# Optimization experiments

Hardware: AMD Instinct MI355X
Metric: run time of the kernel (lower is better)

Reference implementation:

```python
import jax, jax.numpy as jnp
import numpy as np

T, B, D, H, L = 512, 64, 1024, 1024, 2
W_SCALE = 0.02  # keep tanh out of saturation


def setup_inputs() -> dict:
    key = jax.random.key(0)
    ks = jax.random.split(key, 7)
    return {
        "x": jax.random.normal(ks[0], (T, B, D), dtype=jnp.float32),
        "Wi": jax.random.normal(ks[1], (L, H, D), dtype=jnp.float32) * W_SCALE,
        "bi": jax.random.normal(ks[2], (L, H), dtype=jnp.float32) * W_SCALE,
        "Wh": jax.random.normal(ks[3], (L, H, H), dtype=jnp.float32) * W_SCALE,
        "bh": jax.random.normal(ks[4], (L, H), dtype=jnp.float32) * W_SCALE,
        "Wo": jax.random.normal(ks[5], (L, H, H), dtype=jnp.float32) * W_SCALE,
        "bo": jax.random.normal(ks[6], (L, H), dtype=jnp.float32) * W_SCALE,
    }


def reference(x, Wi, bi, Wh, bh, Wo, bo):
    # Faithful to the original: ONE hidden state shared across all layers,
    # overwritten by each RNNCell call within a timestep.
    num_layers = Wi.shape[0]
    batch = x.shape[1]
    hidden0 = jnp.zeros((batch, Wh.shape[-1]), dtype=x.dtype)

    def step(hidden, xt):
        out = xt
        for l in range(num_layers):
            # h = i2h(out) + h2h(hidden); o = h2o(h); new hidden = tanh(h)
            h = out @ Wi[l].T + bi[l] + hidden @ Wh[l].T + bh[l]  # [B,H]
            out = h @ Wo[l].T + bo[l]
            hidden = jnp.tanh(h)
        return hidden, out

    final_hidden, outs = jax.lax.scan(step, hidden0, x)  # outs: [T,B,H]
    return outs, final_hidden
```

## Files before the change

### kernel.cpp

```cpp
#include <hip/hip_runtime.h>
#include <cstdint>
#include <cstddef>

#define TT   512
#define NWG  256
#define SLOT 65536
#define SLOTB 262144
#define FINALOFF ((size_t)TT * (size_t)SLOT)

#define OFF_M     0
#define OFF_H0    2097152
#define OFF_TH0   (OFF_H0 + 131072)
#define OFF_TH1   (OFF_TH0 + 131072)
#define OFF_H1A   (OFF_TH1 + 131072)
#define OFF_H1B   (OFF_H1A + 131072)
#define OFF_B0    (OFF_H1B + 131072)
#define OFF_C1    (OFF_B0 + 4096)
#define OFF_FLAGS (OFF_C1 + 4096)

typedef _Float16 f16;
typedef unsigned long long ull;
typedef _Float16 v8h __attribute__((ext_vector_type(8)));
typedef float v4f __attribute__((ext_vector_type(4)));

union U2 { ull u[2]; v8h v; };
union P4 { f16 h[4]; ull u; };

__device__ __forceinline__ void st2(void* p, f16 v) {
  __hip_atomic_store((unsigned short*)p, __builtin_bit_cast(unsigned short, v),
                     __ATOMIC_RELAXED, __HIP_MEMORY_SCOPE_AGENT);
}
__device__ __forceinline__ ull ld8(const void* p) {
  return __hip_atomic_load((const ull*)p, __ATOMIC_RELAXED, __HIP_MEMORY_SCOPE_AGENT);
}
__device__ __forceinline__ void ld_frags(const f16* base, v8h out[8]) {
  ull u0[8], u1[8];
#pragma unroll
  for (int s = 0; s < 8; ++s) { const f16* p = base + s * 32; u0[s] = ld8(p); u1[s] = ld8(p + 4); }
#pragma unroll
  for (int s = 0; s < 8; ++s) { U2 c; c.u[0] = u0[s]; c.u[1] = u1[s]; out[s] = c.v; }
}

__device__ __forceinline__ float rcpf(float x) {
#if __has_builtin(__builtin_amdgcn_rcpf)
  return __builtin_amdgcn_rcpf(x);
#else
  return 1.0f / x;
#endif
}
__device__ __forceinline__ float tanhfast(float x) {
  x = fminf(fmaxf(x, -20.0f), 20.0f);
  const float u = __expf(-2.0f * x);
  return 1.0f - 2.0f * u * rcpf(1.0f + u);
}

__global__ void k_init(unsigned int* flags) {
  flags[threadIdx.x] = 0u;
}

__global__ void k_bias(const float* __restrict__ Wi, const float* __restrict__ bi,
                       const float* __restrict__ bh, const float* __restrict__ bo,
                       float* __restrict__ b0, float* __restrict__ c1) {
  const int i = blockIdx.x * 256 + threadIdx.x;
  const float* row = Wi + 1048576 + (size_t)i * 1024;
  float s = 0.f;
  for (int k = 0; k < 1024; k += 4) {
    const float4 w = *(const float4*)&row[k];
    const float4 v = *(const float4*)&bo[k];
    s += w.x * v.x + w.y * v.y + w.z * v.z + w.w * v.w;
  }
  c1[i] = s + bi[1024 + i] + bh[1024 + i];
  b0[i] = bi[i] + bh[i];
}

__global__ __launch_bounds__(256) void k_gemm_M(const float* __restrict__ Wi,
                                                const float* __restrict__ Wo,
                                                f16* __restrict__ Mh) {
  const float* A = Wi + 1048576;
  const float* B = Wo;
  __shared__ float As[16][68];
  __shared__ float Bs[16][68];
  const int bi = blockIdx.x >> 4, bj = blockIdx.x & 15;
  const int i0 = bi * 64, d0 = bj * 64;
  const int ti = threadIdx.x >> 4, tj = threadIdx.x & 15;
  float acc[4][4] = {};
  for (int kc = 0; kc < 1024; kc += 16) {
    const int r = threadIdx.x >> 2, cg = (threadIdx.x & 3) << 2;
    const float4 av = *(const float4*)&A[(size_t)(i0 + r) * 1024 + kc + cg];
    As[cg + 0][r] = av.x; As[cg + 1][r] = av.y; As[cg + 2][r] = av.z; As[cg + 3][r] = av.w;
    const int c2 = threadIdx.x >> 4, dg = (threadIdx.x & 15) << 2;
    const float4 bv = *(const float4*)&B[(size_t)(kc + c2) * 1024 + d0 + dg];
    *(float4*)&Bs[c2][dg] = bv;
    __syncthreads();
#pragma unroll
    for (int kk = 0; kk < 16; ++kk) {
      float a[4], b[4];
#pragma unroll
      for (int q = 0; q < 4; ++q) { a[q] = As[kk][ti * 4 + q]; b[q] = Bs[kk][tj * 4 + q]; }
#pragma unroll
      for (int p = 0; p < 4; ++p)
#pragma unroll
        for (int q = 0; q < 4; ++q) acc[p][q] += a[p] * b[q];
    }
    __syncthreads();
  }
#pragma unroll
  for (int p = 0; p < 4; ++p)
#pragma unroll
    for (int q = 0; q < 4; ++q)
      Mh[(size_t)(i0 + ti * 4 + p) * 1024 + (size_t)(d0 + tj * 4 + q)] = (f16)acc[p][q];
}

__global__ __launch_bounds__(256, 1) void k_z1(const float* __restrict__ x,
                                               const float* __restrict__ Wi,
                                               const float* __restrict__ b0p,
                                               float* __restrict__ dout) {
  const int t = blockIdx.x;
  const int tid = threadIdx.x, l = tid & 63, w = tid >> 6;
  const int lj = l & 15, lk = l >> 4;
  __shared__ __align__(16) f16 XL[64 * 1032];
  const float* xt = x + (size_t)t * SLOT;
  for (int u = tid; u < 16384; u += 256) {
    const int b = u >> 8, c4 = (u & 255) << 2;
    const float4 v = *(const float4*)&xt[(size_t)b * 1024 + c4];
    P4 p; p.h[0] = (f16)v.x; p.h[1] = (f16)v.y; p.h[2] = (f16)v.z; p.h[3] = (f16)v.w;
    *(ull*)&XL[b * 1032 + c4] = p.u;
  }
  __syncthreads();
  for (int jt = 0; jt < 16; ++jt) {
    const int jb = w * 256 + jt * 16;
    v4f acc[4] = {{0.f,0.f,0.f,0.f},{0.f,0.f,0.f,0.f},{0.f,0.f,0.f,0.f},{0.f,0.f,0.f,0.f}};
    for (int ks = 0; ks < 32; ++ks) {
      const int k0 = ks * 32 + lk * 8;
      const float* p = &Wi[(size_t)(jb + lj) * 1024 + k0];
      const float4 a = *(const float4*)p, b = *(const float4*)(p + 4);
      const v8h wf = {(f16)a.x,(f16)a.y,(f16)a.z,(f16)a.w,
                      (f16)b.x,(f16)b.y,(f16)b.z,(f16)b.w};
#pragma unroll
      for (int bt = 0; bt < 4; ++bt) {
        const v8h xf = *(const v8h*)&XL[(bt * 16 + lj) * 1032 + k0];
        acc[bt] = __builtin_amdgcn_mfma_f32_16x16x32_f16(xf, wf, acc[bt], 0, 0, 0);
      }
    }
    const float bias = b0p[jb + lj];
#pragma unroll
    for (int bt = 0; bt < 4; ++bt)
#pragma unroll
      for (int q = 0; q < 4; ++q) {
        const int b = bt * 16 + lk * 4 + q;
        f16* dst = (f16*)((char*)dout + (size_t)t * SLOTB + (size_t)(b >> 4) * 65536
                          + (size_t)(b & 15) * 2048) + (jb + lj);
        *dst = (f16)(acc[bt][q] + bias);
      }
  }
}

__global__ __launch_bounds__(256, 1) void k_rnn(
    const float* __restrict__ Wh, const float* __restrict__ Wo,
    const float* __restrict__ bo,
    char* __restrict__ ws, float* __restrict__ dout)
{
  const f16* Mh = (const f16*)(ws + OFF_M);
  f16* h0h  = (f16*)(ws + OFF_H0);
  f16* th0h = (f16*)(ws + OFF_TH0);
  f16* th1h = (f16*)(ws + OFF_TH1);
  f16* h1r[2] = { (f16*)(ws + OFF_H1A), (f16*)(ws + OFF_H1B) };
  const float* c1p = (const float*)(ws + OFF_C1);
  unsigned int* flags = (unsigned int*)(ws + OFF_FLAGS);

  const int wg = blockIdx.x;
  const int bq = wg & 3;
  const int jt = wg >> 2;
  const int j0 = jt * 16;
  const int tid = threadIdx.x;
  const int l = tid & 63, w = tid >> 6;
  const int lj = l & 15, lk = l >> 4;
  const int rb = tid >> 4, rj = tid & 15;
  unsigned int* gf = flags + bq * 64;

  __shared__ __align__(16) char WLb[4 * 32768];
  __shared__ float red[1024];

  {
    const float* srcs[3] = { Wh, Wh + 1048576, Wo + 1048576 };
    const int mi[3] = { 0, 2, 3 };
#pragma unroll
    for (int m = 0; m < 3; ++m) {
      const float* src = srcs[m];
      for (int u = tid; u < 4096; u += 256) {
        const int j = u >> 8, c4 = (u & 255) << 2;
        const float4 v = *(const float4*)&src[(size_t)(j0 + j) * 1024 + c4];
        P4 p; p.h[0] = (f16)v.x; p.h[1] = (f16)v.y; p.h[2] = (f16)v.z; p.h[3] = (f16)v.w;
        *(ull*)(WLb + mi[m] * 32768 + ((c4 >> 3) << 8) + (j << 4) + ((c4 & 4) << 1)) = p.u;
      }
    }
    for (int u = tid; u < 2048; u += 256) {
      const int j = u >> 7, c8 = (u & 127) << 3;
      const v8h mv = *(const v8h*)&Mh[(size_t)(j0 + j) * 1024 + c8];
      *(v8h*)(WLb + 32768 + ((c8 >> 3) << 8) + (j << 4)) = mv;
    }
  }
  const float c1v = c1p[j0 + rj];
  const float bo1v = bo[1024 + j0 + rj];
  __syncthreads();

  const size_t actbase = (size_t)(bq * 16 + lj) * 1024 + (size_t)(w * 256 + lk * 8);
  const int redw = w * 256 + lk * 64 + lj;
  const size_t rdst = (size_t)(bq * 16 + rb) * 1024 + (size_t)(j0 + rj);
  const int fbase = ((w * 32 + lk) << 8) + (lj << 4);

  auto wfrag = [&](int m, int s) -> v8h {
    return *(const v8h*)(WLb + m * 32768 + fbase + (s << 10));
  };
  auto zptr = [&](int t) -> const f16* {
    return (const f16*)((const char*)dout + (size_t)t * SLOTB + (size_t)bq * 65536
                        + (size_t)rb * 2048) + (j0 + rj);
  };
  auto reduce4 = [&](v4f a) -> float {
    __syncthreads();
#pragma unroll
    for (int q = 0; q < 4; ++q) red[redw + q * 16] = a[q];
    __syncthreads();
    return red[tid] + red[256 + tid] + red[512 + tid] + red[768 + tid];
  };
  auto pollge = [&](unsigned int ph) {
    if (tid < 64)
      while (__hip_atomic_load(&gf[tid], __ATOMIC_RELAXED, __HIP_MEMORY_SCOPE_AGENT) < ph)
        __builtin_amdgcn_s_sleep(1);
    __syncthreads();
    asm volatile("" ::: "memory");
  };
  auto setflag = [&](unsigned int ph) {
    if (tid == 0)
      __hip_atomic_store(&gf[jt], ph, __ATOMIC_RELAXED, __HIP_MEMORY_SCOPE_AGENT);
  };

  float zv = (float)(*zptr(0));
  v8h thf[8];

  for (int t = 0; t < TT; ++t) {
    const bool R = (t > 0);

    v4f accA = {0.f, 0.f, 0.f, 0.f};
    if (R) {
#pragma unroll
      for (int s = 0; s < 8; ++s)
        accA = __builtin_amdgcn_mfma_f32_16x16x32_f16(thf[s], wfrag(0, s), accA, 0, 0, 0);
    }
    const float h0 = reduce4(accA) + zv;
    st2(&h0h[rdst], (f16)h0);
    st2(&th0h[rdst], (f16)tanhfast(h0));

    v8h hrf[8];
    if (R) ld_frags(h1r[(t - 1) & 1] + actbase, hrf);
    float zn = 0.f;
    if (t + 1 < TT) zn = (float)(*zptr(t + 1));

    if (t == 0)            { asm volatile("s_waitcnt vmcnt(1)"  ::: "memory"); }
    else if (t == TT - 1)  { asm volatile("s_waitcnt vmcnt(16)" ::: "memory"); }
    else                   { asm volatile("s_waitcnt vmcnt(17)" ::: "memory"); }
    __syncthreads();
    setflag(2u * t + 1u);

    float oval = 0.f;
    if (R) {
      asm volatile("s_waitcnt vmcnt(0)" ::: "memory");
      v4f aa = {0.f, 0.f, 0.f, 0.f};
#pragma unroll
      for (int s = 0; s < 8; ++s)
        aa = __builtin_amdgcn_mfma_f32_16x16x32_f16(hrf[s], wfrag(3, s), aa, 0, 0, 0);
      oval = reduce4(aa) + bo1v;
    }
    pollge(2u * t + 1u);

    v8h g0f[8], t0f[8];
    ld_frags(h0h + actbase, g0f);
    ld_frags(th0h + actbase, t0f);
    v4f aM = {0.f, 0.f, 0.f, 0.f}, aW = {0.f, 0.f, 0.f, 0.f};
#pragma unroll
    for (int s = 0; s < 8; ++s) {
      aM = __builtin_amdgcn_mfma_f32_16x16x32_f16(g0f[s], wfrag(1, s), aM, 0, 0, 0);
      aW = __builtin_amdgcn_mfma_f32_16x16x32_f16(t0f[s], wfrag(2, s), aW, 0, 0, 0);
    }
    const float h1 = reduce4(aM + aW) + c1v;
    const float th1v = tanhfast(h1);
    st2(&h1r[t & 1][rdst], (f16)h1);
    st2(&th1h[rdst], (f16)th1v);
    if (R) dout[(size_t)(t - 1) * SLOT + rdst] = oval;
    if (t == TT - 1) dout[FINALOFF + rdst] = th1v;

    if (t == 0)            { asm volatile("s_waitcnt vmcnt(0)" ::: "memory"); }
    else if (t == TT - 1)  { asm volatile("s_waitcnt vmcnt(2)" ::: "memory"); }
    else                   { asm volatile("s_waitcnt vmcnt(1)" ::: "memory"); }
    __syncthreads();
    setflag(2u * t + 2u);
    pollge(2u * t + 2u);

    if (t + 1 < TT) ld_frags(th1h + actbase, thf);
    zv = zn;
  }

  {
    v8h hrf[8];
    ld_frags(h1r[(TT - 1) & 1] + actbase, hrf);
    v4f aa = {0.f, 0.f, 0.f, 0.f};
#pragma unroll
    for (int s = 0; s < 8; ++s)
      aa = __builtin_amdgcn_mfma_f32_16x16x32_f16(hrf[s], wfrag(3, s), aa, 0, 0, 0);
    dout[(size_t)(TT - 1) * SLOT + rdst] = reduce4(aa) + bo1v;
  }
}

extern "C" void kernel_launch(void* const* d_in, const int* in_sizes, int n_in,
                              void* d_out, int out_size, void* d_ws, size_t ws_size,
                              hipStream_t stream) {
  (void)in_sizes; (void)n_in; (void)out_size; (void)ws_size;
  const float* x  = (const float*)d_in[0];
  const float* Wi = (const float*)d_in[1];
  const float* bi = (const float*)d_in[2];
  const float* Wh = (const float*)d_in[3];
  const float* bh = (const float*)d_in[4];
  const float* Wo = (const float*)d_in[5];
  const float* bo = (const float*)d_in[6];
  char* ws = (char*)d_ws;
  float* out = (float*)d_out;

  k_init<<<1, 256, 0, stream>>>((unsigned int*)(ws + OFF_FLAGS));
  k_bias<<<4, 256, 0, stream>>>(Wi, bi, bh, bo, (float*)(ws + OFF_B0), (float*)(ws + OFF_C1));
  k_gemm_M<<<256, 256, 0, stream>>>(Wi, Wo, (f16*)(ws + OFF_M));
  k_z1<<<512, 256, 0, stream>>>(x, Wi, (const float*)(ws + OFF_B0), out);
  k_rnn<<<NWG, 256, 0, stream>>>(Wh, Wo, bo, ws, out);
}
```

Measured before the change: 6.856 ms.

## Replace flag barriers with tagged fp16 data polling and double-buffered activations

Drops the per-group flag arrays and the two flag-based barrier phases per timestep. Each fp16 activation now carries a 2-bit timestep tag in its low mantissa bits, and consumers spin on the data itself until every fragment holds the expected tag. Activation buffers are double-buffered and initialised to an invalid tag, and the output projection store moves earlier. This removes the global flag round trips and the __syncthreads/flag latency on the recurrent critical path, at the cost of two mantissa bits of precision and heavier polling traffic.

```diff
diff --git a/kernel.cpp b/kernel.cpp
--- a/kernel.cpp
+++ b/kernel.cpp
@@ -8,15 +8,11 @@
 #define SLOTB 262144
 #define FINALOFF ((size_t)TT * (size_t)SLOT)
 
-#define OFF_M     0
-#define OFF_H0    2097152
-#define OFF_TH0   (OFF_H0 + 131072)
-#define OFF_TH1   (OFF_TH0 + 131072)
-#define OFF_H1A   (OFF_TH1 + 131072)
-#define OFF_H1B   (OFF_H1A + 131072)
-#define OFF_B0    (OFF_H1B + 131072)
-#define OFF_C1    (OFF_B0 + 4096)
-#define OFF_FLAGS (OFF_C1 + 4096)
+#define OFF_M    0
+#define OFF_X    2097152
+#define XB(i)    (OFF_X + (i) * 131072)
+#define OFF_B0   (OFF_X + 1048576)
+#define OFF_C1   (OFF_B0 + 4096)
 
 typedef _Float16 f16;
 typedef unsigned long long ull;
@@ -33,12 +29,11 @@
 __device__ __forceinline__ ull ld8(const void* p) {
   return __hip_atomic_load((const ull*)p, __ATOMIC_RELAXED, __HIP_MEMORY_SCOPE_AGENT);
 }
-__device__ __forceinline__ void ld_frags(const f16* base, v8h out[8]) {
-  ull u0[8], u1[8];
-#pragma unroll
-  for (int s = 0; s < 8; ++s) { const f16* p = base + s * 32; u0[s] = ld8(p); u1[s] = ld8(p + 4); }
-#pragma unroll
-  for (int s = 0; s < 8; ++s) { U2 c; c.u[0] = u0[s]; c.u[1] = u1[s]; out[s] = c.v; }
+
+__device__ __forceinline__ f16 tagf(float v, unsigned tag) {
+  unsigned short b = __builtin_bit_cast(unsigned short, (f16)v);
+  b = (unsigned short)((b & 0xFFFCu) | (tag & 3u));
+  return __builtin_bit_cast(f16, b);
 }
 
 __device__ __forceinline__ float rcpf(float x) {
@@ -54,8 +49,9 @@
   return 1.0f - 2.0f * u * rcpf(1.0f + u);
 }
 
-__global__ void k_init(unsigned int* flags) {
-  flags[threadIdx.x] = 0u;
+__global__ void k_init(uint2* p) {
+  const uint2 v = { 0x00020002u, 0x00020002u };
+  p[(size_t)blockIdx.x * 256 + threadIdx.x] = v;
 }
 
 __global__ void k_bias(const float* __restrict__ Wi, const float* __restrict__ bi,
@@ -161,12 +157,11 @@
     char* __restrict__ ws, float* __restrict__ dout)
 {
   const f16* Mh = (const f16*)(ws + OFF_M);
-  f16* h0h  = (f16*)(ws + OFF_H0);
-  f16* th0h = (f16*)(ws + OFF_TH0);
-  f16* th1h = (f16*)(ws + OFF_TH1);
-  f16* h1r[2] = { (f16*)(ws + OFF_H1A), (f16*)(ws + OFF_H1B) };
+  f16* h0b[2]  = { (f16*)(ws + XB(0)), (f16*)(ws + XB(1)) };
+  f16* th0b[2] = { (f16*)(ws + XB(2)), (f16*)(ws + XB(3)) };
+  f16* h1b[2]  = { (f16*)(ws + XB(4)), (f16*)(ws + XB(5)) };
+  f16* th1b[2] = { (f16*)(ws + XB(6)), (f16*)(ws + XB(7)) };
   const float* c1p = (const float*)(ws + OFF_C1);
-  unsigned int* flags = (unsigned int*)(ws + OFF_FLAGS);
 
   const int wg = blockIdx.x;
   const int bq = wg & 3;
@@ -176,7 +171,6 @@
   const int l = tid & 63, w = tid >> 6;
   const int lj = l & 15, lk = l >> 4;
   const int rb = tid >> 4, rj = tid & 15;
-  unsigned int* gf = flags + bq * 64;
 
   __shared__ __align__(16) char WLb[4 * 32768];
   __shared__ float red[1024];
@@ -223,59 +217,80 @@
     __syncthreads();
     return red[tid] + red[256 + tid] + red[512 + tid] + red[768 + tid];
   };
-  auto pollge = [&](unsigned int ph) {
-    if (tid < 64)
-      while (__hip_atomic_load(&gf[tid], __ATOMIC_RELAXED, __HIP_MEMORY_SCOPE_AGENT) < ph)
-        __builtin_amdgcn_s_sleep(1);
-    __syncthreads();
-    asm volatile("" ::: "memory");
-  };
-  auto setflag = [&](unsigned int ph) {
-    if (tid == 0)
-      __hip_atomic_store(&gf[jt], ph, __ATOMIC_RELAXED, __HIP_MEMORY_SCOPE_AGENT);
+
+  auto pollfr = [&](const f16* base, unsigned tag, v8h out[8]) {
+    const ull mask = 0x0003000300030003ULL;
+    const ull expv = 0x0001000100010001ULL * (ull)(tag & 3u);
+    ull u0[8], u1[8];
+    for (;;) {
+#pragma unroll
+      for (int s = 0; s < 8; ++s) { u0[s] = ld8(base + s * 32); u1[s] = ld8(base + s * 32 + 4); }
+      int ok = 1;
+#pragma unroll
+      for (int s = 0; s < 8; ++s)
+        ok &= ((u0[s] & mask) == expv) & ((u1[s] & mask) == expv);
+      if (__all(ok)) break;
+    }
+#pragma unroll
+    for (int s = 0; s < 8; ++s) { U2 c; c.u[0] = u0[s]; c.u[1] = u1[s]; out[s] = c.v; }
+  };
+  auto pollfr2 = [&](const f16* bA, const f16* bB, unsigned tag, v8h oA[8], v8h oB[8]) {
+    const ull mask = 0x0003000300030003ULL;
+    const ull expv = 0x0001000100010001ULL * (ull)(tag & 3u);
+    ull a0[8], a1[8], b0_[8], b1_[8];
+    for (;;) {
+#pragma unroll
+      for (int s = 0; s < 8; ++s) {
+        a0[s] = ld8(bA + s * 32); a1[s] = ld8(bA + s * 32 + 4);
+        b0_[s] = ld8(bB + s * 32); b1_[s] = ld8(bB + s * 32 + 4);
+      }
+      int ok = 1;
+#pragma unroll
+      for (int s = 0; s < 8; ++s) {
+        ok &= ((a0[s] & mask) == expv) & ((a1[s] & mask) == expv);
+        ok &= ((b0_[s] & mask) == expv) & ((b1_[s] & mask) == expv);
+      }
+      if (__all(ok)) break;
+    }
+#pragma unroll
+    for (int s = 0; s < 8; ++s) {
+      U2 c; c.u[0] = a0[s]; c.u[1] = a1[s]; oA[s] = c.v;
+      U2 d; d.u[0] = b0_[s]; d.u[1] = b1_[s]; oB[s] = d.v;
+    }
   };
 
   float zv = (float)(*zptr(0));
-  v8h thf[8];
 
   for (int t = 0; t < TT; ++t) {
     const bool R = (t > 0);
+    const unsigned tg = (unsigned)t & 3u;
 
     v4f accA = {0.f, 0.f, 0.f, 0.f};
     if (R) {
+      v8h thf[8];
+      pollfr(th1b[(t - 1) & 1] + actbase, (unsigned)(t - 1) & 3u, thf);
 #pragma unroll
       for (int s = 0; s < 8; ++s)
         accA = __builtin_amdgcn_mfma_f32_16x16x32_f16(thf[s], wfrag(0, s), accA, 0, 0, 0);
     }
     const float h0 = reduce4(accA) + zv;
-    st2(&h0h[rdst], (f16)h0);
-    st2(&th0h[rdst], (f16)tanhfast(h0));
-
-    v8h hrf[8];
-    if (R) ld_frags(h1r[(t - 1) & 1] + actbase, hrf);
+    st2(&h0b[t & 1][rdst], tagf(h0, tg));
+    st2(&th0b[t & 1][rdst], tagf(tanhfast(h0), tg));
+
     float zn = 0.f;
     if (t + 1 < TT) zn = (float)(*zptr(t + 1));
-
-    if (t == 0)            { asm volatile("s_waitcnt vmcnt(1)"  ::: "memory"); }
-    else if (t == TT - 1)  { asm volatile("s_waitcnt vmcnt(16)" ::: "memory"); }
-    else                   { asm volatile("s_waitcnt vmcnt(17)" ::: "memory"); }
-    __syncthreads();
-    setflag(2u * t + 1u);
-
-    float oval = 0.f;
     if (R) {
-      asm volatile("s_waitcnt vmcnt(0)" ::: "memory");
+      v8h hrf[8];
+      pollfr(h1b[(t - 1) & 1] + actbase, (unsigned)(t - 1) & 3u, hrf);
       v4f aa = {0.f, 0.f, 0.f, 0.f};
 #pragma unroll
       for (int s = 0; s < 8; ++s)
         aa = __builtin_amdgcn_mfma_f32_16x16x32_f16(hrf[s], wfrag(3, s), aa, 0, 0, 0);
-      oval = reduce4(aa) + bo1v;
-    }
-    pollge(2u * t + 1u);
+      dout[(size_t)(t - 1) * SLOT + rdst] = reduce4(aa) + bo1v;
+    }
 
     v8h g0f[8], t0f[8];
-    ld_frags(h0h + actbase, g0f);
-    ld_frags(th0h + actbase, t0f);
+    pollfr2(h0b[t & 1] + actbase, th0b[t & 1] + actbase, tg, g0f, t0f);
     v4f aM = {0.f, 0.f, 0.f, 0.f}, aW = {0.f, 0.f, 0.f, 0.f};
 #pragma unroll
     for (int s = 0; s < 8; ++s) {
@@ -284,25 +299,15 @@
     }
     const float h1 = reduce4(aM + aW) + c1v;
     const float th1v = tanhfast(h1);
-    st2(&h1r[t & 1][rdst], (f16)h1);
-    st2(&th1h[rdst], (f16)th1v);
-    if (R) dout[(size_t)(t - 1) * SLOT + rdst] = oval;
+    st2(&h1b[t & 1][rdst], tagf(h1, tg));
+    st2(&th1b[t & 1][rdst], tagf(th1v, tg));
     if (t == TT - 1) dout[FINALOFF + rdst] = th1v;
-
-    if (t == 0)            { asm volatile("s_waitcnt vmcnt(0)" ::: "memory"); }
-    else if (t == TT - 1)  { asm volatile("s_waitcnt vmcnt(2)" ::: "memory"); }
-    else                   { asm volatile("s_waitcnt vmcnt(1)" ::: "memory"); }
-    __syncthreads();
-    setflag(2u * t + 2u);
-    pollge(2u * t + 2u);
-
-    if (t + 1 < TT) ld_frags(th1h + actbase, thf);
     zv = zn;
   }
 
   {
     v8h hrf[8];
-    ld_frags(h1r[(TT - 1) & 1] + actbase, hrf);
+    pollfr(h1b[(TT - 1) & 1] + actbase, (unsigned)(TT - 1) & 3u, hrf);
     v4f aa = {0.f, 0.f, 0.f, 0.f};
 #pragma unroll
     for (int s = 0; s < 8; ++s)
@@ -325,7 +330,7 @@
   char* ws = (char*)d_ws;
   float* out = (float*)d_out;
 
-  k_init<<<1, 256, 0, stream>>>((unsigned int*)(ws + OFF_FLAGS));
+  k_init<<<512, 256, 0, stream>>>((uint2*)(ws + OFF_X));
   k_bias<<<4, 256, 0, stream>>>(Wi, bi, bh, bo, (float*)(ws + OFF_B0), (float*)(ws + OFF_C1));
   k_gemm_M<<<256, 256, 0, stream>>>(Wi, Wo, (f16*)(ws + OFF_M));
   k_z1<<<512, 256, 0, stream>>>(x, Wi, (const float*)(ws + OFF_B0), out);
```

Result: faster. 6.402 ms (-6.6%).
